# Kernel optimization log

Measured on AMD Instinct MI355X. Metric: run time of the kernel, lower is better.

Reference implementation:

```python
import jax, jax.numpy as jnp
import numpy as np

B, TV, F, H, V, NSTEPS = 64, 40, 2048, 1024, 32000, 30


def setup_inputs() -> dict:
    key = jax.random.key(0)
    ks = jax.random.split(key, 26)
    s = 0.02
    return {
        "batch_size": B,
        "action_feat": jax.random.normal(ks[0], (B, TV, F), jnp.float32),
        "imagenet_feat": jax.random.normal(ks[1], (B, TV, F), jnp.float32),
        "video_mask": jnp.ones((B, TV), jnp.float32),
        "captions": jax.random.randint(ks[2], (B, NSTEPS + 1), 0, V),
        "caption_mask": jnp.ones((B, NSTEPS + 1), jnp.float32),
        "enc_img_W": jax.random.normal(ks[3], (F, H), jnp.float32) * s,
        "enc_img_b": jax.random.normal(ks[4], (H,), jnp.float32) * s,
        "enc_mean_W": jax.random.normal(ks[5], (F, H), jnp.float32) * s,
        "enc_mean_b": jax.random.normal(ks[6], (H,), jnp.float32) * s,
        "att_w": jax.random.normal(ks[7], (H,), jnp.float32) * s,
        "att_Wa": jax.random.normal(ks[8], (H, H), jnp.float32) * s,
        "att_Ua": jax.random.normal(ks[9], (H, H), jnp.float32) * s,
        "att_ba": jax.random.normal(ks[10], (H,), jnp.float32) * s,
        "Wemb": jax.random.normal(ks[11], (V, H), jnp.float32) * s,
        "embed_word_W": jax.random.normal(ks[12], (H, V), jnp.float32) * s,
        "embed_word_b": jax.random.normal(ks[13], (V,), jnp.float32) * s,
        "lstm1_Wih": jax.random.normal(ks[14], (4 * H, 2 * H), jnp.float32) * s,
        "lstm1_Whh": jax.random.normal(ks[15], (4 * H, H), jnp.float32) * s,
        "lstm1_bih": jax.random.normal(ks[16], (4 * H,), jnp.float32) * s,
        "lstm1_bhh": jax.random.normal(ks[17], (4 * H,), jnp.float32) * s,
        "lstm2_Wih": jax.random.normal(ks[18], (4 * H, H), jnp.float32) * s,
        "lstm2_Whh": jax.random.normal(ks[19], (4 * H, H), jnp.float32) * s,
        "lstm2_bih": jax.random.normal(ks[20], (4 * H,), jnp.float32) * s,
        "lstm2_bhh": jax.random.normal(ks[21], (4 * H,), jnp.float32) * s,
    }


def _lstm_cell(x, h, c, Wih, Whh, bih, bhh):
    # PyTorch LSTMCell: gates in order (i, f, g, o)
    g = x @ Wih.T + bih + h @ Whh.T + bhh
    i, f, gg, o = jnp.split(g, 4, axis=-1)
    c_new = jax.nn.sigmoid(f) * c + jax.nn.sigmoid(i) * jnp.tanh(gg)
    h_new = jax.nn.sigmoid(o) * jnp.tanh(c_new)
    return h_new, c_new


def reference(batch_size, action_feat, imagenet_feat, video_mask, captions,
              caption_mask, enc_img_W, enc_img_b, enc_mean_W, enc_mean_b,
              att_w, att_Wa, att_Ua, att_ba, Wemb, embed_word_W, embed_word_b,
              lstm1_Wih, lstm1_Whh, lstm1_bih, lstm1_bhh,
              lstm2_Wih, lstm2_Whh, lstm2_bih, lstm2_bhh):
    bsz = action_feat.shape[0]
    # source code overwrites cat(action, imagenet) with action_feat alone
    video_feat = action_feat @ enc_img_W + enc_img_b          # [B, Tv, H]
    vid_emb = jnp.transpose(video_feat, (1, 0, 2))            # [Tv, B, H]
    feat_mean = jnp.mean(action_feat, axis=1)                 # [B, F]
    feat_mean = feat_mean @ enc_mean_W + enc_mean_b           # [B, H]

    image_part = jnp.einsum('tbh,hk->tbk', vid_emb, att_Ua) + att_ba  # [Tv,B,H]
    vm = video_mask.T                                         # [Tv, B]

    n = captions.shape[1] - 1
    emb_seq = jnp.transpose(Wemb[captions[:, :n]], (1, 0, 2))  # [n, B, H]
    tgts = captions[:, 1:n + 1].T                              # [n, B]
    masks = caption_mask[:, 1:n + 1].T                         # [n, B]

    zeros_h = jnp.zeros((bsz, vid_emb.shape[-1]), jnp.float32)

    def step(carry, xs):
        h1, c1, h2, c2, h_prev, loss = carry
        emb_t, tgt_t, mask_t = xs
        # Bahdanau attention with custom masked softmax
        e = jnp.tanh(h_prev @ att_Wa + image_part)             # [Tv, B, H]
        e = jnp.einsum('tbh,h->tb', e, att_w)                  # [Tv, B]
        e_max = jnp.max(e, axis=0)                             # [B]
        e_hat = vm * jnp.exp(e - e_max)                        # [Tv, B]
        denom = jnp.sum(e_hat, axis=0)
        denom = denom + (denom == 0.0).astype(jnp.float32) + 1e-9
        e_div = e_hat / denom                                  # [Tv, B]
        atten = jnp.einsum('tb,tbh->bh', e_div, vid_emb)       # [B, H]

        x1 = jnp.concatenate([emb_t, atten], axis=1)           # [B, 2H]
        h1, c1 = _lstm_cell(x1, h1, c1, lstm1_Wih, lstm1_Whh, lstm1_bih, lstm1_bhh)
        h2, c2 = _lstm_cell(h1, h2, c2, lstm2_Wih, lstm2_Whh, lstm2_bih, lstm2_bhh)

        logits = h2 @ embed_word_W + embed_word_b              # [B, V]
        logp = jax.nn.log_softmax(logits, axis=-1)
        ce_mean = -jnp.mean(jnp.take_along_axis(logp, tgt_t[:, None], axis=1)[:, 0])
        # original: scalar mean-CE broadcast over mask, summed, / batch_size
        loss = loss + ce_mean * jnp.sum(mask_t) / bsz
        return (h1, c1, h2, c2, h2, loss), None

    init = (feat_mean, zeros_h, zeros_h, zeros_h, feat_mean, jnp.float32(0.0))
    (h1, c1, h2, c2, h_prev, total_loss), _ = jax.lax.scan(
        step, init, (emb_seq, tgts, masks))
    return total_loss
```

## Files before the change

kernel.cpp:

```cpp
#include <hip/hip_runtime.h>
#include <stdint.h>

constexpr int kB   = 64;
constexpr int kTV  = 40;
constexpr int kF   = 2048;
constexpr int kH   = 1024;
constexpr int kV   = 32000;
constexpr int kNS  = 30;
constexpr int kCAP = 31;

typedef __attribute__((ext_vector_type(8))) short bf16x8;
typedef __attribute__((ext_vector_type(4))) float f32x4;
typedef unsigned short us;

__device__ __forceinline__ float sigm(float x) { return 1.f / (1.f + __expf(-x)); }
__device__ __forceinline__ float tanh_fast(float x) {
    float e = __expf(2.f * x);
    return 1.f - 2.f / (e + 1.f);
}
__device__ __forceinline__ us f2bf(float x) {
    unsigned u = __float_as_uint(x);
    return (us)((u + 0x7fffu + ((u >> 16) & 1u)) >> 16);
}
__device__ __forceinline__ float bf2f(us u) {
    return __uint_as_float((unsigned)u << 16);
}

__device__ __forceinline__ void gl16(const us* g, us* lds) {
    __builtin_amdgcn_global_load_lds(
        (const __attribute__((address_space(1))) unsigned int*)(g),
        (__attribute__((address_space(3))) unsigned int*)(lds), 16, 0, 0);
}

template <int N>
__device__ __forceinline__ void waitv() {
    asm volatile("s_waitcnt vmcnt(%0)" :: "n"(N) : "memory");
}
__device__ __forceinline__ void barrier_raw() {
    __builtin_amdgcn_s_barrier();
    asm volatile("" ::: "memory");
}

__device__ __forceinline__ void store_packedA(us* base, int row, int col, us v) {
    int kt = col >> 5, kc = col & 31, ms = row >> 4;
    int l = (row & 15) + (((kc >> 2) & 3) << 4);
    int j = (kc & 3) + ((kc >> 4) << 2);
    base[((((size_t)kt * 4 + ms) * 64 + l) << 3) + j] = v;
}

template <int NSPW, int KT>
__device__ __forceinline__ void mfma_kloop(
    const us* __restrict__ Ap, const us* __restrict__ Bp,
    us* Asm, us* Bsm, int w, int l, f32x4 acc[4][NSPW])
{
    constexpr int BSTEP = 2048 * NSPW;
    constexpr int LPT = 1 + NSPW;
    auto stage = [&](int t, int slot) {
        gl16(Ap + (size_t)t * 2048 + w * 512 + l * 8, Asm + slot * 2048 + w * 512);
#pragma unroll
        for (int i = 0; i < NSPW; ++i)
            gl16(Bp + (size_t)t * BSTEP + (w * NSPW + i) * 512 + l * 8,
                 Bsm + slot * BSTEP + (w * NSPW + i) * 512);
    };
    stage(0, 0); stage(1, 1); stage(2, 2);
#pragma unroll 1
    for (int t = 0; t < KT; ++t) {
        int slot = t % 3;
        int rem = KT - 1 - t;
        if (rem >= 2) waitv<2 * LPT>();
        else if (rem == 1) waitv<LPT>();
        else waitv<0>();
        barrier_raw();
        bf16x8 bfr[NSPW], afr[4];
#pragma unroll
        for (int i = 0; i < NSPW; ++i)
            bfr[i] = *(const bf16x8*)(Bsm + slot * BSTEP + ((w * NSPW + i) * 64 + l) * 8);
#pragma unroll
        for (int ms = 0; ms < 4; ++ms)
            afr[ms] = *(const bf16x8*)(Asm + slot * 2048 + (ms * 64 + l) * 8);
#pragma unroll
        for (int ms = 0; ms < 4; ++ms)
#pragma unroll
            for (int i = 0; i < NSPW; ++i)
                acc[ms][i] = __builtin_amdgcn_mfma_f32_16x16x32_bf16(
                    afr[ms], bfr[i], acc[ms][i], 0, 0, 0);
        __builtin_amdgcn_sched_barrier(0);
        barrier_raw();
        if (t + 3 < KT) stage(t + 3, slot);
    }
}

__global__ __launch_bounds__(256) void prep_mean(
    const float* __restrict__ af, float* __restrict__ fm,
    const float* __restrict__ bih1, const float* __restrict__ bhh1,
    const float* __restrict__ bih2, const float* __restrict__ bhh2,
    const float* __restrict__ capmask,
    float* __restrict__ bsum1, float* __restrict__ bsum2, float* __restrict__ msum)
{
    int tid = threadIdx.x;
    if (blockIdx.x < 64) {
        int b = blockIdx.x;
        const float* base = af + (size_t)b * kTV * kF;
        float a[8] = {};
        for (int t = 0; t < kTV; ++t) {
            const float* rp = base + (size_t)t * kF + tid * 8;
            float4 v0 = *(const float4*)rp;
            float4 v1 = *(const float4*)(rp + 4);
            a[0] += v0.x; a[1] += v0.y; a[2] += v0.z; a[3] += v0.w;
            a[4] += v1.x; a[5] += v1.y; a[6] += v1.z; a[7] += v1.w;
        }
        float* op = fm + (size_t)b * kF + tid * 8;
#pragma unroll
        for (int j = 0; j < 8; ++j) op[j] = a[j] * (1.f / kTV);
    } else {
        int g = (blockIdx.x - 64) * 256 + tid;
        if (g < 4096) bsum1[g] = bih1[g] + bhh1[g];
        else if (g < 8192) { int j = g - 4096; bsum2[j] = bih2[j] + bhh2[j]; }
        else if (g < 8192 + kNS) {
            int t = g - 8192;
            float s = 0.f;
            for (int b = 0; b < kB; ++b) s += capmask[b * kCAP + t + 1];
            msum[t] = s;
        }
    }
}

__global__ __launch_bounds__(256) void pack_rm(
    const float* __restrict__ p0, int ld0, int ksplit,
    const float* __restrict__ p1, int ld1,
    int NGRP, int GS, int HS, int KT,
    us* __restrict__ out)
{
    __shared__ us tile[16][136];
    int kb = blockIdx.x * 128;
    int grp = blockIdx.y;
    int row0 = (grp % NGRP) * GS + (grp / NGRP) * HS;
    int tid = threadIdx.x;
    int r = tid >> 5, c4 = (tid & 31) * 4;
#pragma unroll
    for (int pass = 0; pass < 2; ++pass) {
        int rr = r + pass * 8;
        int row = row0 + rr;
        int k = kb + c4;
        float4 v;
        if (k < ksplit) v = *(const float4*)(p0 + (size_t)row * ld0 + k);
        else            v = *(const float4*)(p1 + (size_t)row * ld1 + (k - ksplit));
        ushort4 o; o.x = f2bf(v.x); o.y = f2bf(v.y); o.z = f2bf(v.z); o.w = f2bf(v.w);
        *(ushort4*)&tile[rr][c4] = o;
    }
    __syncthreads();
    int ktl = tid >> 6, l = tid & 63, ul = l & 15, q = (l >> 4) & 3;
    __align__(16) us o2[8];
#pragma unroll
    for (int j = 0; j < 8; ++j) {
        int kc = (j & 3) + q * 4 + ((j >> 2) << 4);
        o2[j] = tile[ul][ktl * 32 + kc];
    }
    int kt = (kb >> 5) + ktl;
    size_t base = (((size_t)(grp / NGRP) * KT + kt) * NGRP + (grp % NGRP)) * 512;
    *(uint4*)(out + base + (size_t)l * 8) = *(const uint4*)o2;
}

__global__ __launch_bounds__(256) void pack_cm(const float* __restrict__ W,
                                               us* __restrict__ out)
{
    __shared__ us tile[32][136];
    int n0 = blockIdx.x * 128, k0 = blockIdx.y * 32;
    int tid = threadIdx.x;
    int r = tid >> 5, c4 = (tid & 31) * 4;
#pragma unroll
    for (int pass = 0; pass < 4; ++pass) {
        int rr = r + pass * 8;
        float4 v = *(const float4*)(W + (size_t)(k0 + rr) * kV + n0 + c4);
        ushort4 o; o.x = f2bf(v.x); o.y = f2bf(v.y); o.z = f2bf(v.z); o.w = f2bf(v.w);
        *(ushort4*)&tile[rr][c4] = o;
    }
    __syncthreads();
    int ns = tid >> 5, lp = (tid & 31) * 2;
    size_t base = (((size_t)blockIdx.x * 32 + blockIdx.y) * 8 + ns) * 512;
    __align__(16) us o2[16];
#pragma unroll
    for (int li = 0; li < 2; ++li) {
        int l = lp + li, ul = l & 15, q = (l >> 4) & 3;
#pragma unroll
        for (int j = 0; j < 8; ++j) {
            int kc = (j & 3) + q * 4 + ((j >> 2) << 4);
            o2[li * 8 + j] = tile[kc][ns * 16 + ul];
        }
    }
    *(uint4*)(out + base + lp * 8) = *(const uint4*)&o2[0];
    *(uint4*)(out + base + lp * 8 + 8) = *(const uint4*)&o2[8];
}

__global__ __launch_bounds__(256) void pack_sm4(
    const float* __restrict__ Wi, const float* __restrict__ Wm,
    const float* __restrict__ Wua, const float* __restrict__ Wa,
    us* __restrict__ oi, us* __restrict__ om,
    us* __restrict__ oua, us* __restrict__ oa)
{
    int bid = blockIdx.x;
    const float* W; us* out; int KT, rel;
    if (bid < 512)       { W = Wi;  out = oi;  KT = 64; rel = bid; }
    else if (bid < 1024) { W = Wm;  out = om;  KT = 64; rel = bid - 512; }
    else if (bid < 1280) { W = Wua; out = oua; KT = 32; rel = bid - 1024; }
    else                 { W = Wa;  out = oa;  KT = 32; rel = bid - 1280; }
    int bx = rel & 7, by = rel >> 3;
    __shared__ us tile[32][136];
    int n0 = bx * 128, k0 = by * 32;
    int tid = threadIdx.x;
    int r = tid >> 5, c4 = (tid & 31) * 4;
#pragma unroll
    for (int pass = 0; pass < 4; ++pass) {
        int rr = r + pass * 8;
        float4 v = *(const float4*)(W + (size_t)(k0 + rr) * 1024 + n0 + c4);
        ushort4 o; o.x = f2bf(v.x); o.y = f2bf(v.y); o.z = f2bf(v.z); o.w = f2bf(v.w);
        *(ushort4*)&tile[rr][c4] = o;
    }
    __syncthreads();
    int ns = tid >> 5, lp = (tid & 31) * 2;
    int nb64 = bx * 2 + (ns >> 2), ns4 = ns & 3;
    size_t base = (((size_t)nb64 * KT + by) * 4 + ns4) * 512;
    __align__(16) us o2[16];
#pragma unroll
    for (int li = 0; li < 2; ++li) {
        int l = lp + li, ul = l & 15, q = (l >> 4) & 3;
#pragma unroll
        for (int j = 0; j < 8; ++j) {
            int kc = (j & 3) + q * 4 + ((j >> 2) << 4);
            o2[li * 8 + j] = tile[kc][ns * 16 + ul];
        }
    }
    *(uint4*)(out + base + lp * 8) = *(const uint4*)&o2[0];
    *(uint4*)(out + base + lp * 8 + 8) = *(const uint4*)&o2[8];
}

__global__ __launch_bounds__(256) void pack_wae(const float* __restrict__ Wa,
                                                us* __restrict__ WaE)
{
    int nb = blockIdx.x >> 4, cb = blockIdx.x & 15;
    int tid = threadIdx.x;
    int ns = tid >> 6, l = tid & 63;
    int ul = l & 15, q = (l >> 4) & 3;
    int col = cb * 64 + ns * 16 + ul;
    __align__(16) us o[8];
#pragma unroll
    for (int j = 0; j < 4; ++j) {
        int k = (j & 3) + q * 4;
        o[j] = f2bf(Wa[(size_t)(nb * 16 + k) * kH + col]);
    }
    o[4] = 0; o[5] = 0; o[6] = 0; o[7] = 0;
    size_t base = (((size_t)(nb * 16 + cb)) * 4 + ns) * 512;
    *(uint4*)(WaE + base + (size_t)l * 8) = *(const uint4*)o;
}

__global__ __launch_bounds__(256) void pack_emb(
    const float* __restrict__ Wemb, const int* __restrict__ captions,
    us* __restrict__ embP)
{
    __shared__ us tile[16][136];
    int rel = blockIdx.x;
    int s = rel / 32, rem = rel % 32;
    int rg = rem & 3, kb8 = rem >> 2;
    int tid = threadIdx.x;
    int r = tid >> 5, c4 = (tid & 31) * 4;
#pragma unroll
    for (int pass = 0; pass < 2; ++pass) {
        int rr = r + pass * 8;
        int b = rg * 16 + rr;
        int word = captions[b * kCAP + s];
        float4 v = *(const float4*)(Wemb + (size_t)word * kH + kb8 * 128 + c4);
        ushort4 o; o.x = f2bf(v.x); o.y = f2bf(v.y); o.z = f2bf(v.z); o.w = f2bf(v.w);
        *(ushort4*)&tile[rr][c4] = o;
    }
    __syncthreads();
    int ktl = tid >> 6, l = tid & 63, ul = l & 15, q = (l >> 4) & 3;
    __align__(16) us o2[8];
#pragma unroll
    for (int j = 0; j < 8; ++j) {
        int kc = (j & 3) + q * 4 + ((j >> 2) << 4);
        o2[j] = tile[ul][ktl * 32 + kc];
    }
    int kt = kb8 * 4 + ktl;
    size_t base = (((size_t)s * 32 + kt) * 4 + rg) * 512;
    *(uint4*)(embP + base + (size_t)l * 8) = *(const uint4*)o2;
}

template <int KT>
__global__ __launch_bounds__(256) void enc_gemm(
    const us* __restrict__ Ap, const us* __restrict__ Bp,
    const float* __restrict__ bias, float* __restrict__ outF,
    us* __restrict__ outP)
{
    __shared__ us Asm[3][2048];
    __shared__ us Bsm[3][2048];
    int tid = threadIdx.x, w = tid >> 6, l = tid & 63;
    int nb = blockIdx.x, mb = blockIdx.y;
    f32x4 acc[4][1] = {};
    mfma_kloop<1, KT>(Ap + (size_t)mb * KT * 2048, Bp + (size_t)nb * KT * 2048,
                      &Asm[0][0], &Bsm[0][0], w, l, acc);
    int ul = l & 15, sg = l >> 4;
    int n = nb * 64 + w * 16 + ul;
    float bv = bias[n];
#pragma unroll
    for (int ms = 0; ms < 4; ++ms)
#pragma unroll
        for (int r = 0; r < 4; ++r) {
            int rl = ms * 16 + sg * 4 + r;
            int row = mb * 64 + rl;
            float v = acc[ms][0][r] + bv;
            outF[(size_t)row * kH + n] = v;
            if (outP) store_packedA(outP + (size_t)mb * 65536, rl, n, f2bf(v));
        }
}

__global__ __launch_bounds__(256) void p3_gemm(
    const us* __restrict__ Ap, const us* __restrict__ Bp,
    const float* __restrict__ bias, us* __restrict__ xcat1p,
    us* __restrict__ h2hist0)
{
    __shared__ us Asm[3][2048];
    __shared__ us Bsm[3][2048];
    int tid = threadIdx.x, w = tid >> 6, l = tid & 63;
    int nb = blockIdx.x;
    f32x4 acc[4][1] = {};
    mfma_kloop<1, 64>(Ap, Bp + (size_t)nb * 64 * 2048, &Asm[0][0], &Bsm[0][0], w, l, acc);
    int ul = l & 15, sg = l >> 4;
    int n = nb * 64 + w * 16 + ul;
    float bv = bias[n];
#pragma unroll
    for (int ms = 0; ms < 4; ++ms)
#pragma unroll
        for (int r = 0; r < 4; ++r) {
            int row = ms * 16 + sg * 4 + r;
            us hb = f2bf(acc[ms][0][r] + bv);
            store_packedA(xcat1p, row, 1024 + n, hb);
            store_packedA(h2hist0, row, n, hb);
        }
}

__global__ __launch_bounds__(256) void gemb_gemm(
    const us* __restrict__ embP, const us* __restrict__ W1p,
    us* __restrict__ Gemb)
{
    __shared__ us Asm[3][2048];
    __shared__ us Bsm[3][2048];
    int rel = blockIdx.x;
    int s = rel >> 6, nb = rel & 63;
    int tid = threadIdx.x, w = tid >> 6, l = tid & 63;
    f32x4 acc[4][1] = {};
    mfma_kloop<1, 32>(embP + (size_t)s * 65536, W1p + (size_t)nb * 96 * 2048,
                      &Asm[0][0], &Bsm[0][0], w, l, acc);
    int ul = l & 15, sg = l >> 4;
    int n = nb * 64 + w * 16 + ul;
#pragma unroll
    for (int ms = 0; ms < 4; ++ms)
#pragma unroll
        for (int r = 0; r < 4; ++r) {
            int row = ms * 16 + sg * 4 + r;
            Gemb[((size_t)s * 64 + row) * 4096 + n] = f2bf(acc[ms][0][r]);
        }
}

__global__ __launch_bounds__(512) void hwa_gemm(
    const us* __restrict__ h2p, const us* __restrict__ WaP,
    float* __restrict__ hw)
{
    __shared__ __align__(16) char smem[49152];
    float* rsum = (float*)smem;
    int tid = threadIdx.x, w = tid >> 6, l = tid & 63, nb = blockIdx.x;
    int h = w >> 2, w4 = w & 3;
    us* Asm = (us*)(smem + h * 24576);
    us* Bsm = Asm + 6144;
    f32x4 acc[4][1] = {};
    mfma_kloop<1, 16>(h2p + (size_t)h * 16 * 2048,
                      WaP + (size_t)nb * 32 * 2048 + (size_t)h * 16 * 2048,
                      Asm, Bsm, w4, l, acc);
    int ul = l & 15, sg = l >> 4;
    __syncthreads();
    if (h == 1) {
#pragma unroll
        for (int ms = 0; ms < 4; ++ms)
#pragma unroll
            for (int r = 0; r < 4; ++r)
                rsum[((w4 * 64) + ms * 16 + sg * 4 + r) * 17 + ul] = acc[ms][0][r];
    }
    __syncthreads();
    if (h == 0) {
        int n = nb * 64 + w4 * 16 + ul;
#pragma unroll
        for (int ms = 0; ms < 4; ++ms)
#pragma unroll
            for (int r = 0; r < 4; ++r) {
                int row = ms * 16 + sg * 4 + r;
                hw[(size_t)row * kH + n] =
                    acc[ms][0][r] + rsum[((w4 * 64) + row) * 17 + ul];
            }
    }
}

__global__ __launch_bounds__(256) void attn_fused(
    const float* __restrict__ hw0, const float* __restrict__ hwP,
    const float* __restrict__ imgp, const float* __restrict__ attw,
    const float* __restrict__ vf, const float* __restrict__ vmask,
    us* __restrict__ xcat1p)
{
    __shared__ float hwv[kH];
    __shared__ float es[48];
    int b = blockIdx.x, tid = threadIdx.x;
    if (hw0) {
        for (int i = tid; i < kH; i += 256) hwv[i] = hw0[(size_t)b * kH + i];
    } else {
        int c4 = tid * 4;
        float4 a = {0.f, 0.f, 0.f, 0.f};
        for (int nb = 0; nb < 64; ++nb) {
            float4 v = *(const float4*)(hwP + ((size_t)nb * 64 + b) * 1024 + c4);
            a.x += v.x; a.y += v.y; a.z += v.z; a.w += v.w;
        }
        *(float4*)&hwv[c4] = a;
    }
    __syncthreads();
    int w = tid >> 6, l = tid & 63;
    for (int t = w; t < kTV; t += 4) {
        const float* ip = imgp + ((size_t)b * kTV + t) * kH;
        float p = 0.f;
#pragma unroll
        for (int hh = 0; hh < 16; ++hh) {
            int h = hh * 64 + l;
            p += tanh_fast(hwv[h] + ip[h]) * attw[h];
        }
        for (int off = 32; off; off >>= 1) p += __shfl_down(p, off);
        if (l == 0) es[t] = p;
    }
    __syncthreads();
    float mx = -1e30f;
    for (int t = 0; t < kTV; ++t) mx = fmaxf(mx, es[t]);
    const float* vm = vmask + b * kTV;
    float den = 0.f;
    for (int t = 0; t < kTV; ++t) den += vm[t] * __expf(es[t] - mx);
    den = den + (den == 0.f ? 1.f : 0.f) + 1e-9f;
    int h0 = tid * 4;
    float4 av = {0.f, 0.f, 0.f, 0.f};
    for (int t = 0; t < kTV; ++t) {
        float wgt = vm[t] * __expf(es[t] - mx) / den;
        float4 v = *(const float4*)(vf + ((size_t)b * kTV + t) * kH + h0);
        av.x += wgt * v.x; av.y += wgt * v.y; av.z += wgt * v.z; av.w += wgt * v.w;
    }
    store_packedA(xcat1p, b, h0 + 0, f2bf(av.x));
    store_packedA(xcat1p, b, h0 + 1, f2bf(av.y));
    store_packedA(xcat1p, b, h0 + 2, f2bf(av.z));
    store_packedA(xcat1p, b, h0 + 3, f2bf(av.w));
}

template <int KT, int BSTR, int KOFF>
__global__ __launch_bounds__(1024) void gates_cell(
    const us* __restrict__ Ap, const us* __restrict__ Bp,
    const float* __restrict__ bsum, const us* __restrict__ gemb,
    float* __restrict__ cbuf,
    us* __restrict__ dA, int ofsA, us* __restrict__ dB, int ofsB)
{
    __shared__ __align__(16) char smem[98304];
    float* gsm = (float*)smem;
    constexpr int KQ = KT / 4;
    int tid = threadIdx.x, w16 = tid >> 6, l = tid & 63, nb = blockIdx.x;
    int g = w16 >> 2, w4 = w16 & 3;
    us* Asm = (us*)(smem + g * 24576);
    us* Bsm = Asm + 6144;
    f32x4 acc[4][1] = {};
    mfma_kloop<1, KQ>(Ap + (size_t)g * KQ * 2048,
                      Bp + (size_t)nb * BSTR * 2048 + (size_t)(KOFF + g * KQ) * 2048,
                      Asm, Bsm, w4, l, acc);
    int ul = l & 15, sg = l >> 4;
    int sl = (g & 1) * 4 + w4;
    float bv = (g == 0) ? bsum[w4 * 1024 + nb * 16 + ul] : 0.f;
    __syncthreads();
    if (g < 2) {
#pragma unroll
        for (int ms = 0; ms < 4; ++ms)
#pragma unroll
            for (int r = 0; r < 4; ++r)
                gsm[(sl * 64 + ms * 16 + sg * 4 + r) * 17 + ul] = acc[ms][0][r] + bv;
    }
    __syncthreads();
    if (g >= 2) {
#pragma unroll
        for (int ms = 0; ms < 4; ++ms)
#pragma unroll
            for (int r = 0; r < 4; ++r)
                gsm[(sl * 64 + ms * 16 + sg * 4 + r) * 17 + ul] += acc[ms][0][r];
    }
    __syncthreads();
    {
        int row = tid >> 4, uc = tid & 15, u = nb * 16 + uc;
        float ge0 = 0.f, ge1 = 0.f, ge2 = 0.f, ge3 = 0.f;
        if (gemb) {
            const us* gp = gemb + (size_t)row * 4096 + nb * 64 + uc;
            ge0 = bf2f(gp[0]); ge1 = bf2f(gp[16]);
            ge2 = bf2f(gp[32]); ge3 = bf2f(gp[48]);
        }
        float gi = gsm[((0 * 64) + row) * 17 + uc] + gsm[((4 * 64) + row) * 17 + uc] + ge0;
        float gf = gsm[((1 * 64) + row) * 17 + uc] + gsm[((5 * 64) + row) * 17 + uc] + ge1;
        float gg = gsm[((2 * 64) + row) * 17 + uc] + gsm[((6 * 64) + row) * 17 + uc] + ge2;
        float go = gsm[((3 * 64) + row) * 17 + uc] + gsm[((7 * 64) + row) * 17 + uc] + ge3;
        float c = sigm(gf) * cbuf[(size_t)row * kH + u] + sigm(gi) * tanh_fast(gg);
        cbuf[(size_t)row * kH + u] = c;
        us hb = f2bf(sigm(go) * tanh_fast(c));
        store_packedA(dA, row, ofsA + u, hb);
        store_packedA(dB, row, ofsB + u, hb);
    }
}

__global__ __launch_bounds__(1024) void gates2_cell(
    const us* __restrict__ Ap, const us* __restrict__ Bp,
    const float* __restrict__ bsum, float* __restrict__ cbuf,
    us* __restrict__ dA, int ofsA, us* __restrict__ dB, int ofsB,
    float* __restrict__ hwPart, const us* __restrict__ WaE)
{
    __shared__ __align__(16) char smem[98304];
    float* gsm = (float*)smem;
    us* hA = (us*)(smem + 40960);
    constexpr int KQ = 16;
    int tid = threadIdx.x, w16 = tid >> 6, l = tid & 63, nb = blockIdx.x;
    int g = w16 >> 2, w4 = w16 & 3;
    us* Asm = (us*)(smem + g * 24576);
    us* Bsm = Asm + 6144;
    f32x4 acc[4][1] = {};
    mfma_kloop<1, KQ>(Ap + (size_t)g * KQ * 2048,
                      Bp + (size_t)nb * 64 * 2048 + (size_t)(g * KQ) * 2048,
                      Asm, Bsm, w4, l, acc);
    int ul = l & 15, sg = l >> 4;
    int sl = (g & 1) * 4 + w4;
    float bv = (g == 0) ? bsum[w4 * 1024 + nb * 16 + ul] : 0.f;
    __syncthreads();
    if (g < 2) {
#pragma unroll
        for (int ms = 0; ms < 4; ++ms)
#pragma unroll
            for (int r = 0; r < 4; ++r)
                gsm[(sl * 64 + ms * 16 + sg * 4 + r) * 17 + ul] = acc[ms][0][r] + bv;
    }
    __syncthreads();
    if (g >= 2) {
#pragma unroll
        for (int ms = 0; ms < 4; ++ms)
#pragma unroll
            for (int r = 0; r < 4; ++r)
                gsm[(sl * 64 + ms * 16 + sg * 4 + r) * 17 + ul] += acc[ms][0][r];
    }
    __syncthreads();
    int row = tid >> 4, uc = tid & 15, u = nb * 16 + uc;
    {
        float gi = gsm[((0 * 64) + row) * 17 + uc] + gsm[((4 * 64) + row) * 17 + uc];
        float gf = gsm[((1 * 64) + row) * 17 + uc] + gsm[((5 * 64) + row) * 17 + uc];
        float gg = gsm[((2 * 64) + row) * 17 + uc] + gsm[((6 * 64) + row) * 17 + uc];
        float go = gsm[((3 * 64) + row) * 17 + uc] + gsm[((7 * 64) + row) * 17 + uc];
        float c = sigm(gf) * cbuf[(size_t)row * kH + u] + sigm(gi) * tanh_fast(gg);
        cbuf[(size_t)row * kH + u] = c;
        us hb = f2bf(sigm(go) * tanh_fast(c));
        store_packedA(dA, row, ofsA + u, hb);
        store_packedA(dB, row, ofsB + u, hb);
        if (hwPart) {
            *(unsigned*)(hA + tid * 2) = 0;
            __syncthreads();
            int lpos = (row & 15) + (((uc >> 2) & 3) << 4);
            hA[((((row >> 4) * 64) + lpos) << 3) + (uc & 3)] = hb;
            __syncthreads();
            int cb = w16;
            f32x4 hacc[4][4] = {};
            bf16x8 afr[4];
#pragma unroll
            for (int ms = 0; ms < 4; ++ms)
                afr[ms] = *(const bf16x8*)(hA + (ms * 64 + l) * 8);
#pragma unroll
            for (int ns = 0; ns < 4; ++ns) {
                bf16x8 bfr = *(const bf16x8*)(WaE +
                    ((((size_t)(nb * 16 + cb)) * 4 + ns) << 9) + l * 8);
#pragma unroll
                for (int ms = 0; ms < 4; ++ms)
                    hacc[ms][ns] = __builtin_amdgcn_mfma_f32_16x16x32_bf16(
                        afr[ms], bfr, hacc[ms][ns], 0, 0, 0);
            }
#pragma unroll
            for (int ms = 0; ms < 4; ++ms)
#pragma unroll
                for (int ns = 0; ns < 4; ++ns)
#pragma unroll
                    for (int r = 0; r < 4; ++r) {
                        int row2 = ms * 16 + sg * 4 + r;
                        int col = cb * 64 + ns * 16 + ul;
                        hwPart[((size_t)nb * 64 + row2) * 1024 + col] = hacc[ms][ns][r];
                    }
        }
    }
}

__global__ __launch_bounds__(256) void logits_sb(
    const us* __restrict__ h2hist, const us* __restrict__ WvP,
    const float* __restrict__ embb, const int* __restrict__ captions,
    float* __restrict__ psumP, float* __restrict__ tlogs)
{
    constexpr int SBLK = 3;
    __shared__ us Asm[SBLK][2][2048];
    __shared__ us Bsm[2][4096];
    __shared__ float rsum[4][64];
    __shared__ int stgt[SBLK][64];
    int bid = blockIdx.x;
    int c = bid & 7, q = bid >> 3;
    int sgrp = q % 10, nb = c + (q / 10) * 8;
    if (nb >= 250) return;
    int s0 = sgrp * SBLK;
    int tid = threadIdx.x, w = tid >> 6, l = tid & 63, ul = l & 15, lsg = l >> 4;
    if (tid < 64)
#pragma unroll
        for (int si = 0; si < SBLK; ++si)
            stgt[si][tid] = captions[tid * kCAP + s0 + si + 1];
    const us* Ab0 = h2hist + (size_t)(s0 + 1) * 65536;
    const us* Ab1 = h2hist + (size_t)(s0 + 2) * 65536;
    const us* Ab2 = h2hist + (size_t)(s0 + 3) * 65536;
    const us* Bb  = WvP + (size_t)nb * 32 * 4096;
    auto stage = [&](int t, int slot) {
        gl16(Ab0 + (size_t)t * 2048 + w * 512 + l * 8, &Asm[0][slot][w * 512]);
        gl16(Ab1 + (size_t)t * 2048 + w * 512 + l * 8, &Asm[1][slot][w * 512]);
        gl16(Ab2 + (size_t)t * 2048 + w * 512 + l * 8, &Asm[2][slot][w * 512]);
#pragma unroll
        for (int i = 0; i < 2; ++i)
            gl16(Bb + (size_t)t * 4096 + (w * 2 + i) * 512 + l * 8,
                 &Bsm[slot][(w * 2 + i) * 512]);
    };
    f32x4 acc[SBLK][4][2] = {};
    stage(0, 0); stage(1, 1);
#pragma unroll 1
    for (int t = 0; t < 32; ++t) {
        int slot = t & 1;
        if (t < 31) waitv<5>();
        else waitv<0>();
        barrier_raw();
        bf16x8 b0 = *(const bf16x8*)&Bsm[slot][((w * 2 + 0) * 64 + l) * 8];
        bf16x8 b1 = *(const bf16x8*)&Bsm[slot][((w * 2 + 1) * 64 + l) * 8];
#pragma unroll
        for (int ms = 0; ms < 4; ++ms)
#pragma unroll
            for (int si = 0; si < SBLK; ++si) {
                bf16x8 a = *(const bf16x8*)&Asm[si][slot][(ms * 64 + l) * 8];
                acc[si][ms][0] = __builtin_amdgcn_mfma_f32_16x16x32_bf16(a, b0, acc[si][ms][0], 0, 0, 0);
                acc[si][ms][1] = __builtin_amdgcn_mfma_f32_16x16x32_bf16(a, b1, acc[si][ms][1], 0, 0, 0);
            }
        __builtin_amdgcn_sched_barrier(0);
        barrier_raw();
        if (t + 2 < 32) stage(t + 2, slot);
    }
    int n0 = nb * 128 + (2 * w + 0) * 16 + ul;
    int n1 = nb * 128 + (2 * w + 1) * 16 + ul;
    float e0 = embb[n0], e1 = embb[n1];
#pragma unroll
    for (int si = 0; si < SBLK; ++si) {
        float ls[4][4];
#pragma unroll
        for (int ms = 0; ms < 4; ++ms)
#pragma unroll
            for (int r = 0; r < 4; ++r) {
                int row = ms * 16 + lsg * 4 + r;
                float v0 = acc[si][ms][0][r] + e0, v1 = acc[si][ms][1][r] + e1;
                ls[ms][r] = __expf(v0) + __expf(v1);
                if (n0 == stgt[si][row]) tlogs[(s0 + si) * 64 + row] = v0;
                if (n1 == stgt[si][row]) tlogs[(s0 + si) * 64 + row] = v1;
            }
#pragma unroll
        for (int m = 1; m < 16; m <<= 1)
#pragma unroll
            for (int ms = 0; ms < 4; ++ms)
#pragma unroll
                for (int r = 0; r < 4; ++r)
                    ls[ms][r] += __shfl_xor(ls[ms][r], m);
        if (ul == 0)
#pragma unroll
            for (int ms = 0; ms < 4; ++ms)
#pragma unroll
                for (int r = 0; r < 4; ++r)
                    rsum[w][ms * 16 + lsg * 4 + r] = ls[ms][r];
        __syncthreads();
        if (tid < 64)
            psumP[((size_t)(s0 + si) * 250 + nb) * 64 + tid] =
                rsum[0][tid] + rsum[1][tid] + rsum[2][tid] + rsum[3][tid];
        __syncthreads();
    }
}

__global__ __launch_bounds__(256) void final_loss(
    const float* __restrict__ psumP, const float* __restrict__ tlogs,
    const float* __restrict__ msum, float* __restrict__ out)
{
    __shared__ float sl[16000];
    int s = blockIdx.x, tid = threadIdx.x;
    const float* src = psumP + (size_t)s * 16000;
    for (int i = tid; i < 16000; i += 256) sl[i] = src[i];
    __syncthreads();
    if (tid < 64) {
        float tot = 0.f;
        for (int i = 0; i < 250; ++i) tot += sl[i * 64 + tid];
        float logp = tlogs[s * 64 + tid] - __logf(tot);
        float term = -logp * msum[s] * (1.f / 4096.f);
        for (int off = 32; off; off >>= 1) term += __shfl_down(term, off);
        if (tid == 0) atomicAdd(out, term);
    }
}

extern "C" void kernel_launch(void* const* d_in, const int* in_sizes, int n_in,
                              void* d_out, int out_size, void* d_ws, size_t ws_size,
                              hipStream_t stream)
{
    const float* action_feat = (const float*)d_in[1];
    const float* video_mask  = (const float*)d_in[3];
    const int*   captions    = (const int*)d_in[4];
    const float* capmask     = (const float*)d_in[5];
    const float* enc_img_W   = (const float*)d_in[6];
    const float* enc_img_b   = (const float*)d_in[7];
    const float* enc_mean_W  = (const float*)d_in[8];
    const float* enc_mean_b  = (const float*)d_in[9];
    const float* att_w       = (const float*)d_in[10];
    const float* att_Wa      = (const float*)d_in[11];
    const float* att_Ua      = (const float*)d_in[12];
    const float* att_ba      = (const float*)d_in[13];
    const float* Wemb        = (const float*)d_in[14];
    const float* embW        = (const float*)d_in[15];
    const float* embb        = (const float*)d_in[16];
    const float* W1ih        = (const float*)d_in[17];
    const float* W1hh        = (const float*)d_in[18];
    const float* b1ih        = (const float*)d_in[19];
    const float* b1hh        = (const float*)d_in[20];
    const float* W2ih        = (const float*)d_in[21];
    const float* W2hh        = (const float*)d_in[22];
    const float* b2ih        = (const float*)d_in[23];
    const float* b2hh        = (const float*)d_in[24];

    char* base = (char*)d_ws;
    size_t off = 0;
    auto alloc = [&](size_t bytes) {
        char* p = base + off;
        off = (off + bytes + 255) & ~(size_t)255;
        return p;
    };
    constexpr int BIG = 0x40000000;

    float* vf    = (float*)alloc((size_t)2560 * 1024 * 4);
    float* imgp  = (float*)alloc((size_t)2560 * 1024 * 4);
    float* fm    = (float*)alloc((size_t)64 * 2048 * 4);
    float* hw    = (float*)alloc((size_t)64 * 1024 * 4);
    float* hwPart= (float*)alloc((size_t)64 * 64 * 1024 * 4);
    float* bsum1 = (float*)alloc(4096 * 4);
    float* bsum2 = (float*)alloc(4096 * 4);
    float* msum  = (float*)alloc(32 * 4);
    float* psumP = (float*)alloc((size_t)kNS * 250 * 64 * 4);
    float* tlogs = (float*)alloc((size_t)kNS * 64 * 4);
    us* Gemb     = (us*)alloc((size_t)kNS * 64 * 4096 * 2);
    us* x2p0 = (us*)alloc((size_t)64 * 2048 * 2);
    us* x2p1 = (us*)alloc((size_t)64 * 2048 * 2);
    float* c1    = (float*)alloc((size_t)64 * 1024 * 4);
    float* c2    = (float*)alloc((size_t)64 * 1024 * 4);
    size_t zlen  = (size_t)((char*)(c2 + 64 * 1024) - (char*)x2p0);

    us* x1p0 = (us*)alloc((size_t)64 * 2048 * 2);
    us* x1p1 = (us*)alloc((size_t)64 * 2048 * 2);
    us* h2hist = (us*)alloc((size_t)(kNS + 1) * 64 * 1024 * 2);
    us* embP = (us*)alloc((size_t)kNS * 64 * 1024 * 2);
    us* afP  = (us*)alloc((size_t)2560 * 2048 * 2);
    us* vfP  = (us*)alloc((size_t)2560 * 1024 * 2);
    us* fmP  = (us*)alloc((size_t)64 * 2048 * 2);
    us* WiP  = (us*)alloc((size_t)2048 * 1024 * 2);
    us* WmP  = (us*)alloc((size_t)2048 * 1024 * 2);
    us* WuaP = (us*)alloc((size_t)1024 * 1024 * 2);
    us* WaP  = (us*)alloc((size_t)1024 * 1024 * 2);
    us* WaE  = (us*)alloc((size_t)64 * 16 * 4 * 512 * 2);
    us* W1p  = (us*)alloc((size_t)3072 * 4096 * 2);
    us* W2p  = (us*)alloc((size_t)2048 * 4096 * 2);
    us* WvP  = (us*)alloc((size_t)1024 * 32000 * 2);
    if (off > ws_size) return;

    hipMemsetAsync(d_out, 0, 4, stream);
    hipMemsetAsync(x2p0, 0, zlen, stream);

    prep_mean<<<97, 256, 0, stream>>>(action_feat, fm, b1ih, b1hh, b2ih, b2hh,
                                      capmask, bsum1, bsum2, msum);
    pack_rm<<<dim3(16, 4), 256, 0, stream>>>(fm, 2048, BIG, nullptr, 0,
                                             4, 16, 64, 64, fmP);
    pack_rm<<<dim3(16, 160), 256, 0, stream>>>(action_feat, 2048, BIG, nullptr, 0,
                                               4, 16, 64, 64, afP);
    pack_rm<<<dim3(24, 256), 256, 0, stream>>>(W1ih, 2048, 2048, W1hh, 1024,
                                               4, 1024, 16, 96, W1p);
    pack_rm<<<dim3(16, 256), 256, 0, stream>>>(W2ih, 1024, 1024, W2hh, 1024,
                                               4, 1024, 16, 64, W2p);
    pack_sm4<<<1536, 256, 0, stream>>>(enc_img_W, enc_mean_W, att_Ua, att_Wa,
                                       WiP, WmP, WuaP, WaP);
    pack_wae<<<1024, 256, 0, stream>>>(att_Wa, WaE);
    pack_cm<<<dim3(250, 32), 256, 0, stream>>>(embW, WvP);
    pack_emb<<<960, 256, 0, stream>>>(Wemb, captions, embP);

    enc_gemm<64><<<dim3(16, 40), 256, 0, stream>>>(afP, WiP, enc_img_b, vf, vfP);
    p3_gemm<<<16, 256, 0, stream>>>(fmP, WmP, enc_mean_b, x1p0, h2hist);
    enc_gemm<32><<<dim3(16, 40), 256, 0, stream>>>(vfP, WuaP, att_ba, imgp, nullptr);
    gemb_gemm<<<1920, 256, 0, stream>>>(embP, W1p, Gemb);
    hwa_gemm<<<16, 512, 0, stream>>>(h2hist, WaP, hw);

    for (int s = 0; s < kNS; ++s) {
        us* x1c = (s & 1) ? x1p1 : x1p0;
        us* x1n = (s & 1) ? x1p0 : x1p1;
        us* x2c = (s & 1) ? x2p1 : x2p0;
        us* x2n = (s & 1) ? x2p0 : x2p1;
        attn_fused<<<64, 256, 0, stream>>>(
            (s == 0) ? hw : nullptr, hwPart, imgp, att_w, vf, video_mask, x1c);
        gates_cell<64, 96, 32><<<64, 1024, 0, stream>>>(
            x1c, W1p, bsum1, Gemb + (size_t)s * 64 * 4096, c1,
            x1n, 1024, x2c, 0);
        gates2_cell<<<64, 1024, 0, stream>>>(
            x2c, W2p, bsum2, c2,
            x2n, 1024, h2hist + (size_t)(s + 1) * 65536, 0,
            (s < kNS - 1) ? hwPart : nullptr, WaE);
    }
    logits_sb<<<2560, 256, 0, stream>>>(h2hist, WvP, embb, captions, psumP, tlogs);
    final_loss<<<kNS, 256, 0, stream>>>(psumP, tlogs, msum, (float*)d_out);
}
```

Baseline: 2.042 ms.

## Store encoder outputs and attention partials in bf16; double k-step in vocab GEMM

```diff
diff --git a/kernel.cpp b/kernel.cpp
--- a/kernel.cpp
+++ b/kernel.cpp
@@ -288,7 +288,7 @@
 template <int KT>
 __global__ __launch_bounds__(256) void enc_gemm(
     const us* __restrict__ Ap, const us* __restrict__ Bp,
-    const float* __restrict__ bias, float* __restrict__ outF,
+    const float* __restrict__ bias, us* __restrict__ outF,
     us* __restrict__ outP)
 {
     __shared__ us Asm[3][2048];
@@ -308,7 +308,7 @@
             int rl = ms * 16 + sg * 4 + r;
             int row = mb * 64 + rl;
             float v = acc[ms][0][r] + bv;
-            outF[(size_t)row * kH + n] = v;
+            outF[(size_t)row * kH + n] = f2bf(v);
             if (outP) store_packedA(outP + (size_t)mb * 65536, rl, n, f2bf(v));
         }
 }
@@ -399,9 +399,9 @@
 }
 
 __global__ __launch_bounds__(256) void attn_fused(
-    const float* __restrict__ hw0, const float* __restrict__ hwP,
-    const float* __restrict__ imgp, const float* __restrict__ attw,
-    const float* __restrict__ vf, const float* __restrict__ vmask,
+    const float* __restrict__ hw0, const us* __restrict__ hwP,
+    const us* __restrict__ imgp, const float* __restrict__ attw,
+    const us* __restrict__ vf, const float* __restrict__ vmask,
     us* __restrict__ xcat1p)
 {
     __shared__ float hwv[kH];
@@ -411,22 +411,22 @@
         for (int i = tid; i < kH; i += 256) hwv[i] = hw0[(size_t)b * kH + i];
     } else {
         int c4 = tid * 4;
-        float4 a = {0.f, 0.f, 0.f, 0.f};
+        float a0 = 0.f, a1 = 0.f, a2 = 0.f, a3 = 0.f;
         for (int nb = 0; nb < 64; ++nb) {
-            float4 v = *(const float4*)(hwP + ((size_t)nb * 64 + b) * 1024 + c4);
-            a.x += v.x; a.y += v.y; a.z += v.z; a.w += v.w;
-        }
-        *(float4*)&hwv[c4] = a;
+            ushort4 v = *(const ushort4*)(hwP + ((size_t)nb * 64 + b) * 1024 + c4);
+            a0 += bf2f(v.x); a1 += bf2f(v.y); a2 += bf2f(v.z); a3 += bf2f(v.w);
+        }
+        hwv[c4 + 0] = a0; hwv[c4 + 1] = a1; hwv[c4 + 2] = a2; hwv[c4 + 3] = a3;
     }
     __syncthreads();
     int w = tid >> 6, l = tid & 63;
     for (int t = w; t < kTV; t += 4) {
-        const float* ip = imgp + ((size_t)b * kTV + t) * kH;
+        const us* ip = imgp + ((size_t)b * kTV + t) * kH;
         float p = 0.f;
 #pragma unroll
         for (int hh = 0; hh < 16; ++hh) {
             int h = hh * 64 + l;
-            p += tanh_fast(hwv[h] + ip[h]) * attw[h];
+            p += tanh_fast(hwv[h] + bf2f(ip[h])) * attw[h];
         }
         for (int off = 32; off; off >>= 1) p += __shfl_down(p, off);
         if (l == 0) es[t] = p;
@@ -439,16 +439,17 @@
     for (int t = 0; t < kTV; ++t) den += vm[t] * __expf(es[t] - mx);
     den = den + (den == 0.f ? 1.f : 0.f) + 1e-9f;
     int h0 = tid * 4;
-    float4 av = {0.f, 0.f, 0.f, 0.f};
+    float a0 = 0.f, a1 = 0.f, a2 = 0.f, a3 = 0.f;
     for (int t = 0; t < kTV; ++t) {
         float wgt = vm[t] * __expf(es[t] - mx) / den;
-        float4 v = *(const float4*)(vf + ((size_t)b * kTV + t) * kH + h0);
-        av.x += wgt * v.x; av.y += wgt * v.y; av.z += wgt * v.z; av.w += wgt * v.w;
-    }
-    store_packedA(xcat1p, b, h0 + 0, f2bf(av.x));
-    store_packedA(xcat1p, b, h0 + 1, f2bf(av.y));
-    store_packedA(xcat1p, b, h0 + 2, f2bf(av.z));
-    store_packedA(xcat1p, b, h0 + 3, f2bf(av.w));
+        ushort4 v = *(const ushort4*)(vf + ((size_t)b * kTV + t) * kH + h0);
+        a0 += wgt * bf2f(v.x); a1 += wgt * bf2f(v.y);
+        a2 += wgt * bf2f(v.z); a3 += wgt * bf2f(v.w);
+    }
+    store_packedA(xcat1p, b, h0 + 0, f2bf(a0));
+    store_packedA(xcat1p, b, h0 + 1, f2bf(a1));
+    store_packedA(xcat1p, b, h0 + 2, f2bf(a2));
+    store_packedA(xcat1p, b, h0 + 3, f2bf(a3));
 }
 
 template <int KT, int BSTR, int KOFF>
@@ -513,7 +514,7 @@
     const us* __restrict__ Ap, const us* __restrict__ Bp,
     const float* __restrict__ bsum, float* __restrict__ cbuf,
     us* __restrict__ dA, int ofsA, us* __restrict__ dB, int ofsB,
-    float* __restrict__ hwPart, const us* __restrict__ WaE)
+    us* __restrict__ hwPart, const us* __restrict__ WaE)
 {
     __shared__ __align__(16) char smem[98304];
     float* gsm = (float*)smem;
@@ -587,7 +588,8 @@
                     for (int r = 0; r < 4; ++r) {
                         int row2 = ms * 16 + sg * 4 + r;
                         int col = cb * 64 + ns * 16 + ul;
-                        hwPart[((size_t)nb * 64 + row2) * 1024 + col] = hacc[ms][ns][r];
+                        hwPart[((size_t)nb * 64 + row2) * 1024 + col] =
+                            f2bf(hacc[ms][ns][r]);
                     }
         }
     }
@@ -599,8 +601,8 @@
     float* __restrict__ psumP, float* __restrict__ tlogs)
 {
     constexpr int SBLK = 3;
-    __shared__ us Asm[SBLK][2][2048];
-    __shared__ us Bsm[2][4096];
+    __shared__ us Asm[SBLK][2][4096];
+    __shared__ us Bsm[2][8192];
     __shared__ float rsum[4][64];
     __shared__ int stgt[SBLK][64];
     int bid = blockIdx.x;
@@ -617,36 +619,48 @@
     const us* Ab1 = h2hist + (size_t)(s0 + 2) * 65536;
     const us* Ab2 = h2hist + (size_t)(s0 + 3) * 65536;
     const us* Bb  = WvP + (size_t)nb * 32 * 4096;
-    auto stage = [&](int t, int slot) {
-        gl16(Ab0 + (size_t)t * 2048 + w * 512 + l * 8, &Asm[0][slot][w * 512]);
-        gl16(Ab1 + (size_t)t * 2048 + w * 512 + l * 8, &Asm[1][slot][w * 512]);
-        gl16(Ab2 + (size_t)t * 2048 + w * 512 + l * 8, &Asm[2][slot][w * 512]);
-#pragma unroll
-        for (int i = 0; i < 2; ++i)
-            gl16(Bb + (size_t)t * 4096 + (w * 2 + i) * 512 + l * 8,
-                 &Bsm[slot][(w * 2 + i) * 512]);
+    auto stage = [&](int it, int slot) {
+#pragma unroll
+        for (int kk = 0; kk < 2; ++kk) {
+            int t = it * 2 + kk;
+            gl16(Ab0 + (size_t)t * 2048 + w * 512 + l * 8,
+                 &Asm[0][slot][kk * 2048 + w * 512]);
+            gl16(Ab1 + (size_t)t * 2048 + w * 512 + l * 8,
+                 &Asm[1][slot][kk * 2048 + w * 512]);
+            gl16(Ab2 + (size_t)t * 2048 + w * 512 + l * 8,
+                 &Asm[2][slot][kk * 2048 + w * 512]);
+#pragma unroll
+            for (int i = 0; i < 2; ++i)
+                gl16(Bb + (size_t)t * 4096 + (w * 2 + i) * 512 + l * 8,
+                     &Bsm[slot][kk * 4096 + (w * 2 + i) * 512]);
+        }
     };
     f32x4 acc[SBLK][4][2] = {};
     stage(0, 0); stage(1, 1);
 #pragma unroll 1
-    for (int t = 0; t < 32; ++t) {
-        int slot = t & 1;
-        if (t < 31) waitv<5>();
+    for (int it = 0; it < 16; ++it) {
+        int slot = it & 1;
+        if (it < 15) waitv<10>();
         else waitv<0>();
         barrier_raw();
-        bf16x8 b0 = *(const bf16x8*)&Bsm[slot][((w * 2 + 0) * 64 + l) * 8];
-        bf16x8 b1 = *(const bf16x8*)&Bsm[slot][((w * 2 + 1) * 64 + l) * 8];
-#pragma unroll
-        for (int ms = 0; ms < 4; ++ms)
-#pragma unroll
-            for (int si = 0; si < SBLK; ++si) {
-                bf16x8 a = *(const bf16x8*)&Asm[si][slot][(ms * 64 + l) * 8];
-                acc[si][ms][0] = __builtin_amdgcn_mfma_f32_16x16x32_bf16(a, b0, acc[si][ms][0], 0, 0, 0);
-                acc[si][ms][1] = __builtin_amdgcn_mfma_f32_16x16x32_bf16(a, b1, acc[si][ms][1], 0, 0, 0);
-            }
+#pragma unroll
+        for (int kk = 0; kk < 2; ++kk) {
+            bf16x8 b0 = *(const bf16x8*)&Bsm[slot][kk * 4096 + ((w * 2 + 0) * 64 + l) * 8];
+            bf16x8 b1 = *(const bf16x8*)&Bsm[slot][kk * 4096 + ((w * 2 + 1) * 64 + l) * 8];
+#pragma unroll
+            for (int ms = 0; ms < 4; ++ms)
+#pragma unroll
+                for (int si = 0; si < SBLK; ++si) {
+                    bf16x8 a = *(const bf16x8*)&Asm[si][slot][kk * 2048 + (ms * 64 + l) * 8];
+                    acc[si][ms][0] = __builtin_amdgcn_mfma_f32_16x16x32_bf16(
+                        a, b0, acc[si][ms][0], 0, 0, 0);
+                    acc[si][ms][1] = __builtin_amdgcn_mfma_f32_16x16x32_bf16(
+                        a, b1, acc[si][ms][1], 0, 0, 0);
+                }
+        }
         __builtin_amdgcn_sched_barrier(0);
         barrier_raw();
-        if (t + 2 < 32) stage(t + 2, slot);
+        if (it + 2 < 16) stage(it + 2, slot);
     }
     int n0 = nb * 128 + (2 * w + 0) * 16 + ul;
     int n1 = nb * 128 + (2 * w + 1) * 16 + ul;
@@ -741,11 +755,11 @@
     };
     constexpr int BIG = 0x40000000;
 
-    float* vf    = (float*)alloc((size_t)2560 * 1024 * 4);
-    float* imgp  = (float*)alloc((size_t)2560 * 1024 * 4);
+    us* vf       = (us*)alloc((size_t)2560 * 1024 * 2);
+    us* imgp     = (us*)alloc((size_t)2560 * 1024 * 2);
     float* fm    = (float*)alloc((size_t)64 * 2048 * 4);
     float* hw    = (float*)alloc((size_t)64 * 1024 * 4);
-    float* hwPart= (float*)alloc((size_t)64 * 64 * 1024 * 4);
+    us* hwPart   = (us*)alloc((size_t)64 * 64 * 1024 * 2);
     float* bsum1 = (float*)alloc(4096 * 4);
     float* bsum2 = (float*)alloc(4096 * 4);
     float* msum  = (float*)alloc(32 * 4);
```

Result: no change. 2.065 ms (+1.2%).
